# Performance work log

Measured on AMD Instinct MI355X. Metric: run time of the kernel, lower is better.

## Reference

```python
import jax, jax.numpy as jnp
import numpy as np

TEMPERATURE = 1.0
B, H, S, D = 2, 16, 2048, 128

def setup_inputs() -> dict:
    key = jax.random.key(0)
    kq, kk, kv = jax.random.split(key, 3)
    q = jax.random.normal(kq, (B, H, S, D), dtype=jnp.float32)
    k = jax.random.normal(kk, (B, H, S, D), dtype=jnp.float32)
    v = jax.random.normal(kv, (B, H, S, D), dtype=jnp.float32)
    alpha = jnp.float32(0.5)  # nn.Parameter(torch.tensor(0.5))
    return {"q": q, "k": k, "v": v, "alpha": alpha}

def reference(q, k, v, alpha):
    # scores: [B,H,S,S]
    scores = jnp.einsum('bhqd,bhkd->bhqk', q, k) / TEMPERATURE
    row_mean = jnp.mean(scores, axis=-1, keepdims=True)  # [B,H,S,1]
    adaptive = alpha * scores + (1.0 - alpha) * row_mean
    attn = jax.nn.softmax(adaptive, axis=-1)
    return jnp.einsum('bhqk,bhkd->bhqd', attn, v)
```

## Files before the change

kernel.cpp:

```cpp
#include <hip/hip_runtime.h>


#define S_LEN 2048
#define HD    128
#define BQ    128
#define BK    64
#define NW    4
#define NT    (S_LEN / BK)
#define TILE_USH 16384

typedef __bf16    bf16x8 __attribute__((ext_vector_type(8)));
typedef __bf16    bf16x4 __attribute__((ext_vector_type(4)));
typedef _Float16  f16x8  __attribute__((ext_vector_type(8)));
typedef float     f32x4  __attribute__((ext_vector_type(4)));

__device__ __forceinline__ unsigned short f2bf(float x) {
  unsigned u = __builtin_bit_cast(unsigned, x);
  u = (u + 0x7FFFu + ((u >> 16) & 1u)) >> 16;
  return (unsigned short)u;
}
__device__ __forceinline__ unsigned short f2h(float x) {
  _Float16 h = (_Float16)x;
  return __builtin_bit_cast(unsigned short, h);
}
__device__ __forceinline__ float fast_exp2(float x) {
#if __has_builtin(__builtin_amdgcn_exp2f)
  return __builtin_amdgcn_exp2f(x);
#else
  return exp2f(x);
#endif
}

__global__ __launch_bounds__(256) void attn_prepass_kernel(
    const float* __restrict__ kg, const float* __restrict__ vg,
    unsigned short* __restrict__ ws) {
  __shared__ float T[64 * 130];
  const int blk  = blockIdx.x;
  const int head = blk >> 5;
  const int kt   = blk & 31;
  const int tid  = threadIdx.x;
  const size_t hoff = (size_t)head * S_LEN * HD;
  const float* kp = kg + hoff + (size_t)kt * BK * HD;
  const float* vp = vg + hoff + (size_t)kt * BK * HD;
  unsigned short* wsK  = ws + (size_t)blk * TILE_USH;
  unsigned short* wsVt = wsK + 8192;

#pragma unroll
  for (int it = 0; it < 4; ++it) {
    int idx = it * 256 + tid;
    int key = idx >> 4;
    int ch  = idx & 15;
    const float* src = kp + key * HD + ch * 8;
    float4 a = *(const float4*)src;
    float4 b = *(const float4*)(src + 4);
    float xs[8] = {a.x, a.y, a.z, a.w, b.x, b.y, b.z, b.w};
    union { unsigned short s[8]; uint4 v; } hi;
#pragma unroll
    for (int j = 0; j < 8; ++j) hi.s[j] = f2h(xs[j]);
    int slot = (ch & 8) | ((ch & 7) ^ (key & 7));
    *(uint4*)&wsK[key * 128 + slot * 8] = hi.v;
  }

#pragma unroll
  for (int it = 0; it < 16; ++it) {
    int idx = it * 256 + tid;
    int key = idx >> 6;
    int c2  = idx & 63;
    float2 a = *(const float2*)(vp + (size_t)key * HD + c2 * 2);
    *(float2*)&T[key * 130 + c2 * 2] = a;
  }
  __syncthreads();

#pragma unroll
  for (int r = 0; r < 4; ++r) {
    int idx = r * 256 + tid;
    int dim = idx >> 3;
    int ch  = idx & 7;
    union { unsigned short s[8]; uint4 v; } gg;
#pragma unroll
    for (int j = 0; j < 8; ++j) gg.s[j] = f2bf(T[(ch * 8 + j) * 130 + dim]);
    int slot = ch ^ (dim & 7);
    *(uint4*)&wsVt[dim * 64 + slot * 8] = gg.v;
  }
}

__device__ __forceinline__ void stage_tile(const unsigned short* __restrict__ wt,
                                           unsigned short* dst, int tid, int w) {
#pragma unroll
  for (int r = 0; r < 8; ++r) {
    const unsigned int* gp = (const unsigned int*)(wt + (size_t)(r * 256 + tid) * 8);
    unsigned short* lp = dst + (size_t)(r * 256 + w * 64) * 8;
    __builtin_amdgcn_global_load_lds(
        (const __attribute__((address_space(1))) unsigned int*)gp,
        (__attribute__((address_space(3))) unsigned int*)lp, 16, 0, 0);
  }
}

__global__ __launch_bounds__(256, 2) void adaptive_attn_kernel(
    const float* __restrict__ qg, const unsigned short* __restrict__ ws,
    const float* __restrict__ alphap, float* __restrict__ out) {
  __shared__ unsigned short sBuf[2][TILE_USH];
  __shared__ unsigned short sP[NW][2][1024];

  const int b    = blockIdx.x;
  const int head = (b & 7) * 4 + ((b >> 3) & 3);
  const int qt   = b >> 5;

  const int tid  = threadIdx.x;
  const int w    = tid >> 6;
  const int lane = tid & 63;
  const int g    = lane >> 4;
  const int qi   = lane & 15;

  const float lscale = alphap[0] * 1.44269504088896f;

  f16x8 qf[2][4];
#pragma unroll
  for (int h = 0; h < 2; ++h) {
    const int qrow = qt * BQ + w * 32 + h * 16 + qi;
    const float* qp = qg + (size_t)head * S_LEN * HD + (size_t)qrow * HD;
#pragma unroll
    for (int c = 0; c < 4; ++c) {
      float4 a  = *(const float4*)(qp + c * 32 + g * 8);
      float4 bb = *(const float4*)(qp + c * 32 + g * 8 + 4);
      float xs[8] = {a.x, a.y, a.z, a.w, bb.x, bb.y, bb.z, bb.w};
      union { f16x8 v; _Float16 s[8]; } hh;
#pragma unroll
      for (int j = 0; j < 8; ++j) hh.s[j] = (_Float16)(xs[j] * lscale);
      qf[h][c] = hh.v;
    }
  }

  f32x4 o[2][8];
#pragma unroll
  for (int h = 0; h < 2; ++h)
#pragma unroll
    for (int dt = 0; dt < 8; ++dt) o[h][dt] = (f32x4){0.f, 0.f, 0.f, 0.f};
  float lrun[2] = {0.f, 0.f};

  bf16x8 vreg[8][2];
  bf16x8 pf[2][2];

  const unsigned short* wsh = ws + (size_t)head * NT * TILE_USH;

  stage_tile(wsh, &sBuf[0][0], tid, w);
  __syncthreads();

  for (int kt = 0; kt < NT; ++kt) {
    const unsigned short* sK  = &sBuf[kt & 1][0];
    const unsigned short* sVt = sK + 8192;

    if (kt + 1 < NT)
      stage_tile(wsh + (size_t)(kt + 1) * TILE_USH, &sBuf[(kt + 1) & 1][0], tid, w);

    f32x4 st[2][4];
    __builtin_amdgcn_s_setprio(1);
#pragma unroll
    for (int mt = 0; mt < 4; ++mt) {
      f32x4 a0 = (f32x4){0.f, 0.f, 0.f, 0.f};
      f32x4 a1 = (f32x4){0.f, 0.f, 0.f, 0.f};
#pragma unroll
      for (int c = 0; c < 4; ++c) {
        int ch   = c * 4 + g;
        int slot = (ch & 8) | ((ch & 7) ^ (qi & 7));
        f16x8 ah = *(const f16x8*)&sK[(mt * 16 + qi) * 128 + slot * 8];
        a0 = __builtin_amdgcn_mfma_f32_16x16x32_f16(ah, qf[0][c], a0, 0, 0, 0);
        a1 = __builtin_amdgcn_mfma_f32_16x16x32_f16(ah, qf[1][c], a1, 0, 0, 0);
      }
      st[0][mt] = a0; st[1][mt] = a1;
    }
    __builtin_amdgcn_s_setprio(0);

    if (kt > 0) {
      __builtin_amdgcn_s_setprio(1);
#pragma unroll
      for (int dt = 0; dt < 8; ++dt) {
        f32x4 a0 = o[0][dt];
        f32x4 a1 = o[1][dt];
#pragma unroll
        for (int c = 0; c < 2; ++c) {
          a0 = __builtin_amdgcn_mfma_f32_16x16x32_bf16(pf[0][c], vreg[dt][c], a0, 0, 0, 0);
          a1 = __builtin_amdgcn_mfma_f32_16x16x32_bf16(pf[1][c], vreg[dt][c], a1, 0, 0, 0);
        }
        o[0][dt] = a0; o[1][dt] = a1;
      }
      __builtin_amdgcn_s_setprio(0);
    }

#pragma unroll
    for (int h = 0; h < 2; ++h) {
      unsigned short* sPh = &sP[w][h][0];
#pragma unroll
      for (int mt = 0; mt < 4; ++mt) {
        float p0 = fast_exp2(st[h][mt][0]);
        float p1 = fast_exp2(st[h][mt][1]);
        float p2 = fast_exp2(st[h][mt][2]);
        float p3 = fast_exp2(st[h][mt][3]);
        lrun[h] += (p0 + p1) + (p2 + p3);
        bf16x4 pv4;
        pv4[0] = (__bf16)p0; pv4[1] = (__bf16)p1;
        pv4[2] = (__bf16)p2; pv4[3] = (__bf16)p3;
        int slot = (mt * 2 + (g >> 1)) ^ (qi & 7);
        *(bf16x4*)&sPh[qi * 64 + slot * 8 + (g & 1) * 4] = pv4;
      }
    }

#pragma unroll
    for (int h = 0; h < 2; ++h)
#pragma unroll
      for (int c = 0; c < 2; ++c) {
        int slot = (c * 4 + g) ^ (qi & 7);
        pf[h][c] = *(const bf16x8*)&sP[w][h][qi * 64 + slot * 8];
      }

#pragma unroll
    for (int dt = 0; dt < 8; ++dt)
#pragma unroll
      for (int c = 0; c < 2; ++c) {
        int slot = (c * 4 + g) ^ (qi & 7);
        vreg[dt][c] = *(const bf16x8*)&sVt[(dt * 16 + qi) * 64 + slot * 8];
      }

    __syncthreads();
  }

  __builtin_amdgcn_s_setprio(1);
#pragma unroll
  for (int dt = 0; dt < 8; ++dt) {
    f32x4 a0 = o[0][dt];
    f32x4 a1 = o[1][dt];
#pragma unroll
    for (int c = 0; c < 2; ++c) {
      a0 = __builtin_amdgcn_mfma_f32_16x16x32_bf16(pf[0][c], vreg[dt][c], a0, 0, 0, 0);
      a1 = __builtin_amdgcn_mfma_f32_16x16x32_bf16(pf[1][c], vreg[dt][c], a1, 0, 0, 0);
    }
    o[0][dt] = a0; o[1][dt] = a1;
  }
  __builtin_amdgcn_s_setprio(0);

  float* oph = out + (size_t)head * S_LEN * HD + (size_t)(qt * BQ + w * 32) * HD;
#pragma unroll
  for (int h = 0; h < 2; ++h) {
    float ltot = lrun[h];
    ltot += __shfl_xor(ltot, 16, 64);
    ltot += __shfl_xor(ltot, 32, 64);
    float inv[4];
#pragma unroll
    for (int r = 0; r < 4; ++r) {
      float lr = __shfl(ltot, g * 4 + r, 64);
      inv[r] = 1.0f / lr;
    }
    float* op = oph + (size_t)(h * 16) * HD;
#pragma unroll
    for (int dt = 0; dt < 8; ++dt) {
#pragma unroll
      for (int r = 0; r < 4; ++r) {
        op[(size_t)(g * 4 + r) * HD + dt * 16 + qi] = o[h][dt][r] * inv[r];
      }
    }
  }
}

extern "C" void kernel_launch(void* const* d_in, const int* in_sizes, int n_in,
                              void* d_out, int out_size, void* d_ws, size_t ws_size,
                              hipStream_t stream) {
  const float* q     = (const float*)d_in[0];
  const float* k     = (const float*)d_in[1];
  const float* v     = (const float*)d_in[2];
  const float* alpha = (const float*)d_in[3];
  float* out = (float*)d_out;
  unsigned short* ws = (unsigned short*)d_ws;

  hipLaunchKernelGGL(attn_prepass_kernel, dim3(1024), dim3(256), 0, stream,
                     k, v, ws);
  hipLaunchKernelGGL(adaptive_attn_kernel, dim3(512), dim3(256), 0, stream,
                     q, ws, alpha, out);
}
```

Baseline: 200.8 us.

## Load V fragments directly from global in MFMA layout, halve query tile

The prepass now writes V in a separate workspace region, pre-arranged in the per-lane MFMA operand layout, so the attention kernel loads V fragments straight from global memory into registers instead of staging them through LDS. Only K is double-buffered in shared memory, which halves LDS use. The query tile shrinks to 64 rows with 2 waves per block and the grid doubles to 1024 blocks. The software-pipelined PV MFMA that used the previous tile's P is replaced by an in-iteration PV step, which exposes global V load latency and the P round-trip within each iteration and doubles how often K and V are re-read per head.

```diff
diff --git a/kernel.cpp b/kernel.cpp
--- a/kernel.cpp
+++ b/kernel.cpp
@@ -3,11 +3,13 @@
 
 #define S_LEN 2048
 #define HD    128
-#define BQ    128
+#define BQ    64
 #define BK    64
-#define NW    4
+#define NW    2
 #define NT    (S_LEN / BK)
-#define TILE_USH 16384
+#define KTILE_USH 8192
+#define VTILE_USH 8192
+#define VBASE_USH (32 * NT * KTILE_USH)
 
 typedef __bf16    bf16x8 __attribute__((ext_vector_type(8)));
 typedef __bf16    bf16x4 __attribute__((ext_vector_type(4)));
@@ -42,8 +44,8 @@
   const size_t hoff = (size_t)head * S_LEN * HD;
   const float* kp = kg + hoff + (size_t)kt * BK * HD;
   const float* vp = vg + hoff + (size_t)kt * BK * HD;
-  unsigned short* wsK  = ws + (size_t)blk * TILE_USH;
-  unsigned short* wsVt = wsK + 8192;
+  unsigned short* wsK = ws + (size_t)blk * KTILE_USH;
+  unsigned short* wsV = ws + VBASE_USH + (size_t)blk * VTILE_USH;
 
 #pragma unroll
   for (int it = 0; it < 4; ++it) {
@@ -79,27 +81,27 @@
     union { unsigned short s[8]; uint4 v; } gg;
 #pragma unroll
     for (int j = 0; j < 8; ++j) gg.s[j] = f2bf(T[(ch * 8 + j) * 130 + dim]);
-    int slot = ch ^ (dim & 7);
-    *(uint4*)&wsVt[dim * 64 + slot * 8] = gg.v;
-  }
-}
-
-__device__ __forceinline__ void stage_tile(const unsigned short* __restrict__ wt,
-                                           unsigned short* dst, int tid, int w) {
+    int gidx = ((dim >> 4) * 2 + (ch >> 2)) * 64 + (ch & 3) * 16 + (dim & 15);
+    *(uint4*)&wsV[gidx * 8] = gg.v;
+  }
+}
+
+__device__ __forceinline__ void stage_k(const unsigned short* __restrict__ wt,
+                                        unsigned short* dst, int tid, int w) {
 #pragma unroll
   for (int r = 0; r < 8; ++r) {
-    const unsigned int* gp = (const unsigned int*)(wt + (size_t)(r * 256 + tid) * 8);
-    unsigned short* lp = dst + (size_t)(r * 256 + w * 64) * 8;
+    const unsigned int* gp = (const unsigned int*)(wt + (size_t)(r * 128 + tid) * 8);
+    unsigned short* lp = dst + (size_t)(r * 128 + w * 64) * 8;
     __builtin_amdgcn_global_load_lds(
         (const __attribute__((address_space(1))) unsigned int*)gp,
         (__attribute__((address_space(3))) unsigned int*)lp, 16, 0, 0);
   }
 }
 
-__global__ __launch_bounds__(256, 2) void adaptive_attn_kernel(
+__global__ __launch_bounds__(128, 2) void adaptive_attn_kernel(
     const float* __restrict__ qg, const unsigned short* __restrict__ ws,
     const float* __restrict__ alphap, float* __restrict__ out) {
-  __shared__ unsigned short sBuf[2][TILE_USH];
+  __shared__ unsigned short sBuf[2][KTILE_USH];
   __shared__ unsigned short sP[NW][2][1024];
 
   const int b    = blockIdx.x;
@@ -138,20 +140,25 @@
     for (int dt = 0; dt < 8; ++dt) o[h][dt] = (f32x4){0.f, 0.f, 0.f, 0.f};
   float lrun[2] = {0.f, 0.f};
 
-  bf16x8 vreg[8][2];
-  bf16x8 pf[2][2];
-
-  const unsigned short* wsh = ws + (size_t)head * NT * TILE_USH;
-
-  stage_tile(wsh, &sBuf[0][0], tid, w);
+  const unsigned short* wsKh = ws + (size_t)head * NT * KTILE_USH;
+  const unsigned short* wsVh = ws + VBASE_USH + (size_t)head * NT * VTILE_USH;
+
+  stage_k(wsKh, &sBuf[0][0], tid, w);
   __syncthreads();
 
   for (int kt = 0; kt < NT; ++kt) {
-    const unsigned short* sK  = &sBuf[kt & 1][0];
-    const unsigned short* sVt = sK + 8192;
+    const unsigned short* sK = &sBuf[kt & 1][0];
+
+    const unsigned short* vb = wsVh + (size_t)kt * VTILE_USH;
+    bf16x8 vf[8][2];
+#pragma unroll
+    for (int dt = 0; dt < 8; ++dt)
+#pragma unroll
+      for (int c = 0; c < 2; ++c)
+        vf[dt][c] = *(const bf16x8*)&vb[((dt * 2 + c) * 64 + lane) * 8];
 
     if (kt + 1 < NT)
-      stage_tile(wsh + (size_t)(kt + 1) * TILE_USH, &sBuf[(kt + 1) & 1][0], tid, w);
+      stage_k(wsKh + (size_t)(kt + 1) * KTILE_USH, &sBuf[(kt + 1) & 1][0], tid, w);
 
     f32x4 st[2][4];
     __builtin_amdgcn_s_setprio(1);
@@ -170,22 +177,6 @@
       st[0][mt] = a0; st[1][mt] = a1;
     }
     __builtin_amdgcn_s_setprio(0);
-
-    if (kt > 0) {
-      __builtin_amdgcn_s_setprio(1);
-#pragma unroll
-      for (int dt = 0; dt < 8; ++dt) {
-        f32x4 a0 = o[0][dt];
-        f32x4 a1 = o[1][dt];
-#pragma unroll
-        for (int c = 0; c < 2; ++c) {
-          a0 = __builtin_amdgcn_mfma_f32_16x16x32_bf16(pf[0][c], vreg[dt][c], a0, 0, 0, 0);
-          a1 = __builtin_amdgcn_mfma_f32_16x16x32_bf16(pf[1][c], vreg[dt][c], a1, 0, 0, 0);
-        }
-        o[0][dt] = a0; o[1][dt] = a1;
-      }
-      __builtin_amdgcn_s_setprio(0);
-    }
 
 #pragma unroll
     for (int h = 0; h < 2; ++h) {
@@ -205,6 +196,7 @@
       }
     }
 
+    bf16x8 pf[2][2];
 #pragma unroll
     for (int h = 0; h < 2; ++h)
 #pragma unroll
@@ -213,30 +205,22 @@
         pf[h][c] = *(const bf16x8*)&sP[w][h][qi * 64 + slot * 8];
       }
 
-#pragma unroll
-    for (int dt = 0; dt < 8; ++dt)
+    __builtin_amdgcn_s_setprio(1);
+#pragma unroll
+    for (int dt = 0; dt < 8; ++dt) {
+      f32x4 a0 = o[0][dt];
+      f32x4 a1 = o[1][dt];
 #pragma unroll
       for (int c = 0; c < 2; ++c) {
-        int slot = (c * 4 + g) ^ (qi & 7);
-        vreg[dt][c] = *(const bf16x8*)&sVt[(dt * 16 + qi) * 64 + slot * 8];
-      }
+        a0 = __builtin_amdgcn_mfma_f32_16x16x32_bf16(pf[0][c], vf[dt][c], a0, 0, 0, 0);
+        a1 = __builtin_amdgcn_mfma_f32_16x16x32_bf16(pf[1][c], vf[dt][c], a1, 0, 0, 0);
+      }
+      o[0][dt] = a0; o[1][dt] = a1;
+    }
+    __builtin_amdgcn_s_setprio(0);
 
     __syncthreads();
   }
-
-  __builtin_amdgcn_s_setprio(1);
-#pragma unroll
-  for (int dt = 0; dt < 8; ++dt) {
-    f32x4 a0 = o[0][dt];
-    f32x4 a1 = o[1][dt];
-#pragma unroll
-    for (int c = 0; c < 2; ++c) {
-      a0 = __builtin_amdgcn_mfma_f32_16x16x32_bf16(pf[0][c], vreg[dt][c], a0, 0, 0, 0);
-      a1 = __builtin_amdgcn_mfma_f32_16x16x32_bf16(pf[1][c], vreg[dt][c], a1, 0, 0, 0);
-    }
-    o[0][dt] = a0; o[1][dt] = a1;
-  }
-  __builtin_amdgcn_s_setprio(0);
 
   float* oph = out + (size_t)head * S_LEN * HD + (size_t)(qt * BQ + w * 32) * HD;
 #pragma unroll
@@ -273,6 +257,6 @@
 
   hipLaunchKernelGGL(attn_prepass_kernel, dim3(1024), dim3(256), 0, stream,
                      k, v, ws);
-  hipLaunchKernelGGL(adaptive_attn_kernel, dim3(512), dim3(256), 0, stream,
+  hipLaunchKernelGGL(adaptive_attn_kernel, dim3(1024), dim3(128), 0, stream,
                      q, ws, alpha, out);
 }
```

Measured after the change: 212.9 us. 6.0% more time.

## Split key tile across wave pairs with halved query block and LDS reduction

Applied to the files above, without the earlier changes.

Halves the query block to 64 rows and doubles the grid. Each pair of waves now shares 32 query rows and splits every 64-key tile, each wave taking 32 keys, with a final LDS reduction of the partial outputs and row sums. It also drops the software-pipelined PV MFMA (deferred P/V registers) and the setprio hints, computing PV inline. The aim is better CU occupancy and lower register pressure, at the cost of K/V tiles being staged twice as often per query row and an extra reduction step.

```diff
diff --git a/kernel.cpp b/kernel.cpp
--- a/kernel.cpp
+++ b/kernel.cpp
@@ -3,9 +3,8 @@
 
 #define S_LEN 2048
 #define HD    128
-#define BQ    128
+#define BQ    64
 #define BK    64
-#define NW    4
 #define NT    (S_LEN / BK)
 #define TILE_USH 16384
 
@@ -100,7 +99,8 @@
     const float* __restrict__ qg, const unsigned short* __restrict__ ws,
     const float* __restrict__ alphap, float* __restrict__ out) {
   __shared__ unsigned short sBuf[2][TILE_USH];
-  __shared__ unsigned short sP[NW][2][1024];
+  __shared__ unsigned short sP[4][2][512];
+  __shared__ float sL[2][2][16];
 
   const int b    = blockIdx.x;
   const int head = (b & 7) * 4 + ((b >> 3) & 3);
@@ -108,6 +108,8 @@
 
   const int tid  = threadIdx.x;
   const int w    = tid >> 6;
+  const int qp   = w >> 1;
+  const int kh   = w & 1;
   const int lane = tid & 63;
   const int g    = lane >> 4;
   const int qi   = lane & 15;
@@ -117,12 +119,12 @@
   f16x8 qf[2][4];
 #pragma unroll
   for (int h = 0; h < 2; ++h) {
-    const int qrow = qt * BQ + w * 32 + h * 16 + qi;
-    const float* qp = qg + (size_t)head * S_LEN * HD + (size_t)qrow * HD;
+    const int qrow = qt * BQ + qp * 32 + h * 16 + qi;
+    const float* qp_ = qg + (size_t)head * S_LEN * HD + (size_t)qrow * HD;
 #pragma unroll
     for (int c = 0; c < 4; ++c) {
-      float4 a  = *(const float4*)(qp + c * 32 + g * 8);
-      float4 bb = *(const float4*)(qp + c * 32 + g * 8 + 4);
+      float4 a  = *(const float4*)(qp_ + c * 32 + g * 8);
+      float4 bb = *(const float4*)(qp_ + c * 32 + g * 8 + 4);
       float xs[8] = {a.x, a.y, a.z, a.w, bb.x, bb.y, bb.z, bb.w};
       union { f16x8 v; _Float16 s[8]; } hh;
 #pragma unroll
@@ -137,9 +139,6 @@
 #pragma unroll
     for (int dt = 0; dt < 8; ++dt) o[h][dt] = (f32x4){0.f, 0.f, 0.f, 0.f};
   float lrun[2] = {0.f, 0.f};
-
-  bf16x8 vreg[8][2];
-  bf16x8 pf[2][2];
 
   const unsigned short* wsh = ws + (size_t)head * NT * TILE_USH;
 
@@ -153,45 +152,28 @@
     if (kt + 1 < NT)
       stage_tile(wsh + (size_t)(kt + 1) * TILE_USH, &sBuf[(kt + 1) & 1][0], tid, w);
 
-    f32x4 st[2][4];
-    __builtin_amdgcn_s_setprio(1);
-#pragma unroll
-    for (int mt = 0; mt < 4; ++mt) {
+    f32x4 st[2][2];
+#pragma unroll
+    for (int mt = 0; mt < 2; ++mt) {
       f32x4 a0 = (f32x4){0.f, 0.f, 0.f, 0.f};
       f32x4 a1 = (f32x4){0.f, 0.f, 0.f, 0.f};
+      const int keyrow = (kh * 2 + mt) * 16 + qi;
 #pragma unroll
       for (int c = 0; c < 4; ++c) {
         int ch   = c * 4 + g;
         int slot = (ch & 8) | ((ch & 7) ^ (qi & 7));
-        f16x8 ah = *(const f16x8*)&sK[(mt * 16 + qi) * 128 + slot * 8];
+        f16x8 ah = *(const f16x8*)&sK[keyrow * 128 + slot * 8];
         a0 = __builtin_amdgcn_mfma_f32_16x16x32_f16(ah, qf[0][c], a0, 0, 0, 0);
         a1 = __builtin_amdgcn_mfma_f32_16x16x32_f16(ah, qf[1][c], a1, 0, 0, 0);
       }
       st[0][mt] = a0; st[1][mt] = a1;
     }
-    __builtin_amdgcn_s_setprio(0);
-
-    if (kt > 0) {
-      __builtin_amdgcn_s_setprio(1);
-#pragma unroll
-      for (int dt = 0; dt < 8; ++dt) {
-        f32x4 a0 = o[0][dt];
-        f32x4 a1 = o[1][dt];
-#pragma unroll
-        for (int c = 0; c < 2; ++c) {
-          a0 = __builtin_amdgcn_mfma_f32_16x16x32_bf16(pf[0][c], vreg[dt][c], a0, 0, 0, 0);
-          a1 = __builtin_amdgcn_mfma_f32_16x16x32_bf16(pf[1][c], vreg[dt][c], a1, 0, 0, 0);
-        }
-        o[0][dt] = a0; o[1][dt] = a1;
-      }
-      __builtin_amdgcn_s_setprio(0);
-    }
 
 #pragma unroll
     for (int h = 0; h < 2; ++h) {
       unsigned short* sPh = &sP[w][h][0];
 #pragma unroll
-      for (int mt = 0; mt < 4; ++mt) {
+      for (int mt = 0; mt < 2; ++mt) {
         float p0 = fast_exp2(st[h][mt][0]);
         float p1 = fast_exp2(st[h][mt][1]);
         float p2 = fast_exp2(st[h][mt][2]);
@@ -200,62 +182,71 @@
         bf16x4 pv4;
         pv4[0] = (__bf16)p0; pv4[1] = (__bf16)p1;
         pv4[2] = (__bf16)p2; pv4[3] = (__bf16)p3;
-        int slot = (mt * 2 + (g >> 1)) ^ (qi & 7);
-        *(bf16x4*)&sPh[qi * 64 + slot * 8 + (g & 1) * 4] = pv4;
-      }
-    }
-
-#pragma unroll
-    for (int h = 0; h < 2; ++h)
-#pragma unroll
-      for (int c = 0; c < 2; ++c) {
-        int slot = (c * 4 + g) ^ (qi & 7);
-        pf[h][c] = *(const bf16x8*)&sP[w][h][qi * 64 + slot * 8];
-      }
-
-#pragma unroll
-    for (int dt = 0; dt < 8; ++dt)
-#pragma unroll
-      for (int c = 0; c < 2; ++c) {
-        int slot = (c * 4 + g) ^ (qi & 7);
-        vreg[dt][c] = *(const bf16x8*)&sVt[(dt * 16 + qi) * 64 + slot * 8];
-      }
+        int slot = (mt * 2 + (g >> 1)) ^ (qi & 3);
+        *(bf16x4*)&sPh[qi * 32 + slot * 8 + (g & 1) * 4] = pv4;
+      }
+    }
+
+    bf16x8 pf[2];
+#pragma unroll
+    for (int h = 0; h < 2; ++h) {
+      int slot = g ^ (qi & 3);
+      pf[h] = *(const bf16x8*)&sP[w][h][qi * 32 + slot * 8];
+    }
+
+#pragma unroll
+    for (int dt = 0; dt < 8; ++dt) {
+      int slot = (kh * 4 + g) ^ (qi & 7);
+      bf16x8 vf = *(const bf16x8*)&sVt[(dt * 16 + qi) * 64 + slot * 8];
+      o[0][dt] = __builtin_amdgcn_mfma_f32_16x16x32_bf16(pf[0], vf, o[0][dt], 0, 0, 0);
+      o[1][dt] = __builtin_amdgcn_mfma_f32_16x16x32_bf16(pf[1], vf, o[1][dt], 0, 0, 0);
+    }
 
     __syncthreads();
   }
 
-  __builtin_amdgcn_s_setprio(1);
-#pragma unroll
-  for (int dt = 0; dt < 8; ++dt) {
-    f32x4 a0 = o[0][dt];
-    f32x4 a1 = o[1][dt];
-#pragma unroll
-    for (int c = 0; c < 2; ++c) {
-      a0 = __builtin_amdgcn_mfma_f32_16x16x32_bf16(pf[0][c], vreg[dt][c], a0, 0, 0, 0);
-      a1 = __builtin_amdgcn_mfma_f32_16x16x32_bf16(pf[1][c], vreg[dt][c], a1, 0, 0, 0);
-    }
-    o[0][dt] = a0; o[1][dt] = a1;
-  }
-  __builtin_amdgcn_s_setprio(0);
-
-  float* oph = out + (size_t)head * S_LEN * HD + (size_t)(qt * BQ + w * 32) * HD;
+  float lt[2];
 #pragma unroll
   for (int h = 0; h < 2; ++h) {
-    float ltot = lrun[h];
-    ltot += __shfl_xor(ltot, 16, 64);
-    ltot += __shfl_xor(ltot, 32, 64);
-    float inv[4];
-#pragma unroll
-    for (int r = 0; r < 4; ++r) {
-      float lr = __shfl(ltot, g * 4 + r, 64);
-      inv[r] = 1.0f / lr;
-    }
-    float* op = oph + (size_t)(h * 16) * HD;
-#pragma unroll
-    for (int dt = 0; dt < 8; ++dt) {
+    float t = lrun[h];
+    t += __shfl_xor(t, 16, 64);
+    t += __shfl_xor(t, 32, 64);
+    lt[h] = t;
+  }
+
+  float* sRed = (float*)&sBuf[0][0];
+  if (kh == 1) {
+#pragma unroll
+    for (int h = 0; h < 2; ++h) {
+#pragma unroll
+      for (int dt = 0; dt < 8; ++dt)
+#pragma unroll
+        for (int r = 0; r < 4; ++r)
+          sRed[qp * 4096 + ((h * 8 + dt) * 4 + r) * 64 + lane] = o[h][dt][r];
+      if (lane < 16) sL[qp][h][qi] = lt[h];
+    }
+  }
+  __syncthreads();
+
+  if (kh == 0) {
+    float* oph = out + (size_t)head * S_LEN * HD + (size_t)(qt * BQ + qp * 32) * HD;
+#pragma unroll
+    for (int h = 0; h < 2; ++h) {
+      float comb = lt[h] + sL[qp][h][qi];
+      float inv[4];
 #pragma unroll
       for (int r = 0; r < 4; ++r) {
-        op[(size_t)(g * 4 + r) * HD + dt * 16 + qi] = o[h][dt][r] * inv[r];
+        float lr = __shfl(comb, g * 4 + r, 64);
+        inv[r] = 1.0f / lr;
+      }
+      float* op = oph + (size_t)(h * 16) * HD;
+#pragma unroll
+      for (int dt = 0; dt < 8; ++dt) {
+#pragma unroll
+        for (int r = 0; r < 4; ++r) {
+          float val = o[h][dt][r] + sRed[qp * 4096 + ((h * 8 + dt) * 4 + r) * 64 + lane];
+          op[(size_t)(g * 4 + r) * HD + dt * 16 + qi] = val * inv[r];
+        }
       }
     }
   }
@@ -273,6 +264,6 @@
 
   hipLaunchKernelGGL(attn_prepass_kernel, dim3(1024), dim3(256), 0, stream,
                      k, v, ws);
-  hipLaunchKernelGGL(adaptive_attn_kernel, dim3(512), dim3(256), 0, stream,
+  hipLaunchKernelGGL(adaptive_attn_kernel, dim3(1024), dim3(256), 0, stream,
                      q, ws, alpha, out);
 }
```

New measurement: 222.2 us. 1.11x slower.

## Keep softmax probabilities in registers via permlane swaps instead of LDS round-trip

Applied to the files above, without the earlier changes.

Converts the exp'd scores to packed bf16 with v_cvt_pk_bf16_f32 and rearranges them into the PV MFMA A-operand layout using permlane32/permlane16 swaps, removing the per-wave sP shared-memory buffer and its write/read. It also drops the one-iteration-delayed PV software pipeline (and the setprio hints), doing PV immediately each tile and loading V fragments inline from LDS. This cuts LDS traffic, LDS footprint and register pressure from vreg buffering, but loses the overlap between the previous tile's PV MFMAs and the current exp work.

```diff
diff --git a/kernel.cpp b/kernel.cpp
--- a/kernel.cpp
+++ b/kernel.cpp
@@ -10,9 +10,10 @@
 #define TILE_USH 16384
 
 typedef __bf16    bf16x8 __attribute__((ext_vector_type(8)));
-typedef __bf16    bf16x4 __attribute__((ext_vector_type(4)));
 typedef _Float16  f16x8  __attribute__((ext_vector_type(8)));
 typedef float     f32x4  __attribute__((ext_vector_type(4)));
+typedef unsigned  uint2v __attribute__((ext_vector_type(2)));
+typedef unsigned  uint4v __attribute__((ext_vector_type(4)));
 
 __device__ __forceinline__ unsigned short f2bf(float x) {
   unsigned u = __builtin_bit_cast(unsigned, x);
@@ -28,6 +29,27 @@
   return __builtin_amdgcn_exp2f(x);
 #else
   return exp2f(x);
+#endif
+}
+__device__ __forceinline__ unsigned cvt_pk_bf16(float lo, float hi) {
+  unsigned r;
+  asm("v_cvt_pk_bf16_f32 %0, %1, %2" : "=v"(r) : "v"(lo), "v"(hi));
+  return r;
+}
+__device__ __forceinline__ void swap32(unsigned &x, unsigned &y) {
+#if __has_builtin(__builtin_amdgcn_permlane32_swap)
+  uint2v r = __builtin_amdgcn_permlane32_swap(x, y, false, false);
+  x = r[0]; y = r[1];
+#else
+  asm("v_permlane32_swap_b32 %0, %1" : "+v"(x), "+v"(y));
+#endif
+}
+__device__ __forceinline__ void swap16(unsigned &x, unsigned &y) {
+#if __has_builtin(__builtin_amdgcn_permlane16_swap)
+  uint2v r = __builtin_amdgcn_permlane16_swap(x, y, false, false);
+  x = r[0]; y = r[1];
+#else
+  asm("v_permlane16_swap_b32 %0, %1" : "+v"(x), "+v"(y));
 #endif
 }
 
@@ -100,7 +122,6 @@
     const float* __restrict__ qg, const unsigned short* __restrict__ ws,
     const float* __restrict__ alphap, float* __restrict__ out) {
   __shared__ unsigned short sBuf[2][TILE_USH];
-  __shared__ unsigned short sP[NW][2][1024];
 
   const int b    = blockIdx.x;
   const int head = (b & 7) * 4 + ((b >> 3) & 3);
@@ -138,9 +159,6 @@
     for (int dt = 0; dt < 8; ++dt) o[h][dt] = (f32x4){0.f, 0.f, 0.f, 0.f};
   float lrun[2] = {0.f, 0.f};
 
-  bf16x8 vreg[8][2];
-  bf16x8 pf[2][2];
-
   const unsigned short* wsh = ws + (size_t)head * NT * TILE_USH;
 
   stage_tile(wsh, &sBuf[0][0], tid, w);
@@ -154,7 +172,6 @@
       stage_tile(wsh + (size_t)(kt + 1) * TILE_USH, &sBuf[(kt + 1) & 1][0], tid, w);
 
     f32x4 st[2][4];
-    __builtin_amdgcn_s_setprio(1);
 #pragma unroll
     for (int mt = 0; mt < 4; ++mt) {
       f32x4 a0 = (f32x4){0.f, 0.f, 0.f, 0.f};
@@ -169,27 +186,11 @@
       }
       st[0][mt] = a0; st[1][mt] = a1;
     }
-    __builtin_amdgcn_s_setprio(0);
-
-    if (kt > 0) {
-      __builtin_amdgcn_s_setprio(1);
-#pragma unroll
-      for (int dt = 0; dt < 8; ++dt) {
-        f32x4 a0 = o[0][dt];
-        f32x4 a1 = o[1][dt];
-#pragma unroll
-        for (int c = 0; c < 2; ++c) {
-          a0 = __builtin_amdgcn_mfma_f32_16x16x32_bf16(pf[0][c], vreg[dt][c], a0, 0, 0, 0);
-          a1 = __builtin_amdgcn_mfma_f32_16x16x32_bf16(pf[1][c], vreg[dt][c], a1, 0, 0, 0);
-        }
-        o[0][dt] = a0; o[1][dt] = a1;
-      }
-      __builtin_amdgcn_s_setprio(0);
-    }
-
+
+    bf16x8 pf[2][2];
 #pragma unroll
     for (int h = 0; h < 2; ++h) {
-      unsigned short* sPh = &sP[w][h][0];
+      unsigned pk[4][2];
 #pragma unroll
       for (int mt = 0; mt < 4; ++mt) {
         float p0 = fast_exp2(st[h][mt][0]);
@@ -197,46 +198,41 @@
         float p2 = fast_exp2(st[h][mt][2]);
         float p3 = fast_exp2(st[h][mt][3]);
         lrun[h] += (p0 + p1) + (p2 + p3);
-        bf16x4 pv4;
-        pv4[0] = (__bf16)p0; pv4[1] = (__bf16)p1;
-        pv4[2] = (__bf16)p2; pv4[3] = (__bf16)p3;
-        int slot = (mt * 2 + (g >> 1)) ^ (qi & 7);
-        *(bf16x4*)&sPh[qi * 64 + slot * 8 + (g & 1) * 4] = pv4;
-      }
-    }
-
-#pragma unroll
-    for (int h = 0; h < 2; ++h)
+        pk[mt][0] = cvt_pk_bf16(p0, p1);
+        pk[mt][1] = cvt_pk_bf16(p2, p3);
+      }
+#pragma unroll
+      for (int c = 0; c < 2; ++c) {
+        uint4v wv;
+#pragma unroll
+        for (int u = 0; u < 2; ++u) {
+          unsigned x = pk[c * 2][u];
+          unsigned y = pk[c * 2 + 1][u];
+          swap32(x, y);
+          swap16(x, y);
+          wv[u]     = x;
+          wv[2 + u] = y;
+        }
+        pf[h][c] = __builtin_bit_cast(bf16x8, wv);
+      }
+    }
+
+#pragma unroll
+    for (int dt = 0; dt < 8; ++dt) {
+      f32x4 a0 = o[0][dt];
+      f32x4 a1 = o[1][dt];
 #pragma unroll
       for (int c = 0; c < 2; ++c) {
         int slot = (c * 4 + g) ^ (qi & 7);
-        pf[h][c] = *(const bf16x8*)&sP[w][h][qi * 64 + slot * 8];
-      }
-
-#pragma unroll
-    for (int dt = 0; dt < 8; ++dt)
-#pragma unroll
-      for (int c = 0; c < 2; ++c) {
-        int slot = (c * 4 + g) ^ (qi & 7);
-        vreg[dt][c] = *(const bf16x8*)&sVt[(dt * 16 + qi) * 64 + slot * 8];
-      }
+        bf16x8 vf = *(const bf16x8*)&sVt[(dt * 16 + qi) * 64 + slot * 8];
+        a0 = __builtin_amdgcn_mfma_f32_16x16x32_bf16(pf[0][c], vf, a0, 0, 0, 0);
+        a1 = __builtin_amdgcn_mfma_f32_16x16x32_bf16(pf[1][c], vf, a1, 0, 0, 0);
+      }
+      o[0][dt] = a0; o[1][dt] = a1;
+    }
 
     __syncthreads();
   }
-
-  __builtin_amdgcn_s_setprio(1);
-#pragma unroll
-  for (int dt = 0; dt < 8; ++dt) {
-    f32x4 a0 = o[0][dt];
-    f32x4 a1 = o[1][dt];
-#pragma unroll
-    for (int c = 0; c < 2; ++c) {
-      a0 = __builtin_amdgcn_mfma_f32_16x16x32_bf16(pf[0][c], vreg[dt][c], a0, 0, 0, 0);
-      a1 = __builtin_amdgcn_mfma_f32_16x16x32_bf16(pf[1][c], vreg[dt][c], a1, 0, 0, 0);
-    }
-    o[0][dt] = a0; o[1][dt] = a1;
-  }
-  __builtin_amdgcn_s_setprio(0);
 
   float* oph = out + (size_t)head * S_LEN * HD + (size_t)(qt * BQ + w * 32) * HD;
 #pragma unroll
```

Measured after the change: 194.4 us. 1.03x faster.
